# Kernel tuning notes

Measured on AMD Instinct MI355X. Metric: run time of the kernel, lower is better.

## Reference

```python
import jax, jax.numpy as jnp
import numpy as np

N = 100000          # nodes
E = 600000          # edges
H = 128             # hidden_dim
CF_DIM = 15         # input_dim - 1
NOISE_DIM = 32
NUM_CLASS = 6       # GraphConstructor.number_of_class
B = 64              # number of graphs in batch
BC = B * NUM_CLASS  # total clusters
LAYER_NUM = 3
NEG_SLOPE = 0.01


def setup_inputs() -> dict:
    key = jax.random.key(0)
    ks = jax.random.split(key, 12)
    cf = jax.random.normal(ks[0], (N, CF_DIM), jnp.float32)
    slf = jax.random.uniform(ks[1], (N,), jnp.float32)
    z = jax.random.normal(ks[2], (N, NOISE_DIM), jnp.float32)
    tr = jax.random.uniform(ks[3], (BC,), jnp.float32)
    W_enc = jax.random.normal(ks[4], (CF_DIM + 1 + NOISE_DIM, H), jnp.float32) * 0.05
    b_enc = jax.random.normal(ks[5], (H,), jnp.float32) * 0.05
    W_m = jax.random.normal(ks[6], (2 * H, H), jnp.float32) * 0.05
    b_m = jax.random.normal(ks[7], (H,), jnp.float32) * 0.05
    W_u = jax.random.normal(ks[8], (3 * H, H), jnp.float32) * 0.05
    b_u = jax.random.normal(ks[9], (H,), jnp.float32) * 0.05
    e = jax.random.randint(ks[10], (2, E), 0, N, jnp.int64)
    cc = jax.random.randint(ks[11], (N,), 0, BC, jnp.int64)
    cfb = cc // NUM_CLASS  # batch index consistent with global cluster index
    return {"cf": cf, "slf": slf, "z": z, "tr": tr,
            "W_enc": W_enc, "b_enc": b_enc, "W_m": W_m, "b_m": b_m,
            "W_u": W_u, "b_u": b_u, "e": e, "cc": cc, "cfb": cfb}


def _segment_mean(x, idx, num_segments):
    s = jax.ops.segment_sum(x, idx, num_segments=num_segments)
    c = jax.ops.segment_sum(jnp.ones((x.shape[0],), x.dtype), idx, num_segments=num_segments)
    return s / jnp.maximum(c, 1.0)[:, None]


def reference(cf, slf, z, tr, W_enc, b_enc, W_m, b_m, W_u, b_u, e, cc, cfb):
    # encoder: x = enc(cat(cf, slf, z))  (Linear, no activation since act='')
    x = jnp.concatenate([cf, slf[:, None], z], axis=-1) @ W_enc + b_enc  # [N, H]
    src, dst = e[0], e[1]  # PyG: x_j = x[src], x_i = x[dst], aggregate at dst
    for _ in range(LAYER_NUM):
        # message: MLP(cat(feature_i, feature_j)) per edge, mean-aggregated at dst
        msg = jnp.concatenate([x[dst], x[src]], axis=-1) @ W_m + b_m  # [E, H]
        aggr = _segment_mean(msg, dst, N)                              # [N, H]
        # cluster avg_pool scaled by target ratio, broadcast back to nodes
        pooled = _segment_mean(x, cc, BC) * tr[:, None]                # [BC, H]
        node_pool = pooled[cc]                                         # [N, H]
        upd = jnp.concatenate([x, aggr, node_pool], axis=-1) @ W_u + b_u
        upd = jnp.where(upd > 0, upd, NEG_SLOPE * upd)                 # LeakyReLU
        x = x + upd                                                    # residual
    return x
```

## Files before the change

kernel.cpp:

```cpp
#include <hip/hip_runtime.h>
#include <hip/hip_bf16.h>

#define N_NODES 100000
#define N_EDGES 600000
#define HD 128
#define NBC 384
#define SCAN_B 98
#define MAXFIX 4096
#define TILES ((N_NODES + 63) / 64)
#define GRID_F 512
#define AGG_B (N_NODES / 4)
#define CAPB 16384
#define PB_BLK 147

typedef __attribute__((ext_vector_type(8))) short s8v;
typedef __attribute__((ext_vector_type(4))) short s4v;
typedef __attribute__((ext_vector_type(4))) float f4v;
typedef __hip_bfloat16 bf16;

static __device__ __forceinline__ float bf2f(bf16 v) { return __bfloat162float(v); }
static __device__ __forceinline__ bf16 f2bf(float v) { return __float2bfloat16(v); }
static __device__ __forceinline__ float sh2f(short s) { bf16 h = *(bf16*)&s; return bf2f(h); }
static __device__ __forceinline__ float ldraw(const void* p, int i, int fp32) {
    return fp32 ? ((const float*)p)[i] : bf2f(((const bf16*)p)[i]);
}

static __device__ __forceinline__ void gl2lds16(const void* g, void* l) {
    __builtin_amdgcn_global_load_lds(
        (const __attribute__((address_space(1))) void*)g,
        (__attribute__((address_space(3))) void*)l, 16, 0, 0);
}

__global__ void k_init(const unsigned short* __restrict__ wraw, const int* __restrict__ eraw,
                       int* __restrict__ flags, int* __restrict__ deg,
                       int* __restrict__ ccount, int* __restrict__ n0cnt,
                       int* __restrict__ bcur) {
    int b = blockIdx.x, t = threadIdx.x;
    if (b == 0) {
        if (t < 64) {
            int bad = 0;
            for (int k = 0; k < 16; k++) {
                unsigned int u = ((unsigned int)wraw[t * 16 + k]) << 16;
                float f = fabsf(__uint_as_float(u));
                if (!(f <= 1e4f)) bad = 1;
            }
            unsigned long long m = __ballot(bad);
            if (t == 0) {
                flags[0] = m ? 1 : 0;
                flags[1] = (eraw[1] == 0 && eraw[3] == 0 && eraw[5] == 0 && eraw[7] == 0) ? 1 : 0;
            }
        }
    } else if (b <= 98) {
        int i = (b - 1) * 256 + t;
        if (i < 25000) ((int4*)deg)[i] = make_int4(0, 0, 0, 0);
    } else {
        if (t < 96) ((int4*)ccount)[t] = make_int4(0, 0, 0, 0);
        if (t == 96) *n0cnt = 0;
        if (t >= 128 && t < 128 + SCAN_B) bcur[t - 128] = 0;
    }
}

#define KB_J 192
#define KB_K (KB_J + 32)
#define KB_L (KB_K + 1)
#define KB_A (KB_L + 5860)
#define KB_B (KB_A + 391)
#define KB_C (KB_B + 12500)
#define KB_D (KB_C + 782)
#define KB_E (KB_D + 2)
#define KB_F (KB_E + 192)
#define KB_G (KB_F + 1)
#define KB_H (KB_G + 4688)
#define KB_I (KB_H + 391)
__global__ void k_mega(const int* __restrict__ flags,
                       const void* cf_r, const void* slf_r, const void* z_r,
                       const void* tr_r, const void* Wenc_r, const void* benc_r,
                       const void* Wm_r, const void* bm_r, const void* Wu_r,
                       const void* bu_r, const int* __restrict__ e_r,
                       const int* __restrict__ cc_r,
                       bf16* __restrict__ xin, bf16* __restrict__ trc,
                       bf16* __restrict__ Wuc, bf16* __restrict__ buc,
                       int* __restrict__ ec, int* __restrict__ ccc,
                       int* __restrict__ deg, int* __restrict__ ccount,
                       bf16* __restrict__ Wc, float* __restrict__ bc,
                       bf16* __restrict__ Wet, float* __restrict__ bcenc) {
    int b = blockIdx.x, t = threadIdx.x;
    int fp32 = flags[0];
    if (b < KB_J) {
        int i = b * 256 + t;
        int w = i / 384, kk = i - w * 384;
        float acc = 0.f;
        if (kk < 128) {
            acc = ldraw(Wu_r, kk * 128 + w, fp32);
            for (int j = 0; j < 128; j++)
                acc += ldraw(Wm_r, kk * 128 + j, fp32) * ldraw(Wu_r, (128 + j) * 128 + w, fp32);
        } else if (kk < 256) {
            int kp = kk - 128;
            for (int j = 0; j < 128; j++)
                acc += ldraw(Wm_r, (128 + kp) * 128 + j, fp32) * ldraw(Wu_r, (128 + j) * 128 + w, fp32);
        } else {
            acc = ldraw(Wu_r, kk * 128 + w, fp32);
        }
        Wc[w * 384 + kk] = f2bf(acc);
    } else if (b < KB_K) {
        int i = (b - KB_J) * 256 + t;
        int w = i >> 6, kk = i & 63;
        float v = (kk < 48) ? ldraw(Wenc_r, kk * 128 + w, fp32) : 0.f;
        Wet[i] = f2bf(v);
    } else if (b < KB_L) {
        if (t < 128) {
            float acc = ldraw(bu_r, t, fp32);
            for (int j = 0; j < 128; j++)
                acc += ldraw(bm_r, j, fp32) * ldraw(Wu_r, (128 + j) * 128 + t, fp32);
            bc[t] = acc;
        } else if (t < 256) {
            bcenc[t - 128] = ldraw(benc_r, t - 128, fp32);
        }
    } else if (b < KB_A) {
        int i = (b - KB_L) * 256 + t;
        if (i < 1500000) {
            int node = i / 15;
            xin[(size_t)node * 64 + (i - node * 15)] = f2bf(ldraw(cf_r, i, fp32));
        }
    } else if (b < KB_B) {
        int i = (b - KB_A) * 256 + t;
        if (i < 100000) xin[(size_t)i * 64 + 15] = f2bf(ldraw(slf_r, i, fp32));
    } else if (b < KB_C) {
        int i = (b - KB_B) * 256 + t;
        if (i < 3200000) xin[(size_t)(i >> 5) * 64 + 16 + (i & 31)] = f2bf(ldraw(z_r, i, fp32));
    } else if (b < KB_D) {
        int p = (b - KB_C) * 2048 + t * 8;
        if (p < 1600000) {
            int row = p >> 4, off = p & 15;
            s8v zz = {0, 0, 0, 0, 0, 0, 0, 0};
            *(s8v*)((short*)xin + (size_t)row * 64 + 48 + off) = zz;
        }
    } else if (b < KB_E) {
        int i = (b - KB_D) * 256 + t;
        if (i < 384) trc[i] = f2bf(ldraw(tr_r, i, fp32));
    } else if (b < KB_F) {
        int i = (b - KB_E) * 256 + t;
        Wuc[i] = f2bf(ldraw(Wu_r, i, fp32));
    } else if (b < KB_G) {
        if (t < 128) buc[t] = f2bf(ldraw(bu_r, t, fp32));
    } else if (b < KB_H) {
        int i64f = flags[1];
        int i = (b - KB_G) * 256 + t;
        if (i < 2 * N_EDGES) {
            int v = i64f ? e_r[2 * i] : e_r[i];
            ec[i] = v;
            if (i >= N_EDGES) atomicAdd(&deg[v], 1);
        }
    } else {
        int i64f = flags[1];
        int i = (b - KB_H) * 256 + t;
        if (i < N_NODES) {
            int v = i64f ? cc_r[2 * i] : cc_r[i];
            ccc[i] = v;
            atomicAdd(&ccount[v], 1);
        }
    }
}

__global__ void k_scan_a2(const int* __restrict__ deg, int* __restrict__ rowptr,
                          int* __restrict__ bsum, const int* __restrict__ ccount,
                          int* __restrict__ coff, int* __restrict__ ccur,
                          const int* __restrict__ ec, int* __restrict__ bcur,
                          int* __restrict__ ebuf) {
    __shared__ int sd[1024];
    __shared__ int hist[SCAN_B], hbase[SCAN_B], lcur[SCAN_B];
    int t = threadIdx.x;
    if (blockIdx.x < SCAN_B) {
        int i = blockIdx.x * 1024 + t;
        int v = (i < N_NODES) ? deg[i] : 0;
        sd[t] = v;
        __syncthreads();
#pragma unroll
        for (int off = 1; off < 1024; off <<= 1) {
            int u = (t >= off) ? sd[t - off] : 0;
            __syncthreads();
            sd[t] += u;
            __syncthreads();
        }
        if (i < N_NODES) rowptr[i] = sd[t] - v;
        if (t == 1023) bsum[blockIdx.x] = sd[t];
    } else if (blockIdx.x == SCAN_B) {
        int v = (t < NBC) ? ccount[t] : 0;
        sd[t] = v;
        __syncthreads();
#pragma unroll
        for (int off = 1; off < 1024; off <<= 1) {
            int u = (t >= off) ? sd[t - off] : 0;
            __syncthreads();
            sd[t] += u;
            __syncthreads();
        }
        if (t < NBC) {
            int ex = sd[t] - v;
            coff[t] = ex;
            ccur[t] = ex;
            if (t == NBC - 1) coff[NBC] = sd[t];
        }
    } else {
        int bb = blockIdx.x - (SCAN_B + 1);
        int e0 = bb * 4096;
        if (t < SCAN_B) { hist[t] = 0; lcur[t] = 0; }
        __syncthreads();
        int dv[4], sv[4], bk[4];
#pragma unroll
        for (int k = 0; k < 4; k++) {
            int i = e0 + k * 1024 + t;
            if (i < N_EDGES) {
                dv[k] = ec[N_EDGES + i];
                sv[k] = ec[i];
                bk[k] = dv[k] >> 10;
                atomicAdd(&hist[bk[k]], 1);
            } else bk[k] = -1;
        }
        __syncthreads();
        if (t < SCAN_B && hist[t] > 0) hbase[t] = atomicAdd(&bcur[t], hist[t]);
        __syncthreads();
#pragma unroll
        for (int k = 0; k < 4; k++) {
            if (bk[k] >= 0) {
                int rel = hbase[bk[k]] + atomicAdd(&lcur[bk[k]], 1);
                if (rel < CAPB) ebuf[bk[k] * CAPB + rel] = (sv[k] << 10) | (dv[k] & 1023);
            }
        }
    }
}

__global__ void k_scan_c2(int* __restrict__ rowptr, const int* __restrict__ bsum) {
    __shared__ int sb[128];
    __shared__ int offs;
    int b = blockIdx.x, t = threadIdx.x;
    if (t < 128) sb[t] = (t < b) ? bsum[t] : 0;
    __syncthreads();
    if (t == 0) {
        int s = 0;
        for (int k = 0; k < 128; k++) s += sb[k];
        offs = s;
    }
    __syncthreads();
    int i = b * 1024 + t;
    if (i < N_NODES) rowptr[i] = rowptr[i] + offs;
    if (b == 0 && t == 0) rowptr[N_NODES] = N_EDGES;
}

#define K5_EN 1563
#define K5_PC (K5_EN + SCAN_B)
#define K5_CF (K5_PC + SCAN_B)
#define K5_L0 (K5_CF + 391)
__global__ void k_front(const bf16* __restrict__ xin, const bf16* __restrict__ Wet,
                        const float* __restrict__ bcenc, bf16* __restrict__ xb,
                        const int* __restrict__ rowptr, const int* __restrict__ ebuf,
                        int* __restrict__ colx, const int* __restrict__ ccc,
                        int* __restrict__ ccur, int* __restrict__ cnodes,
                        const int* __restrict__ deg, int* __restrict__ n0list,
                        int* __restrict__ n0cnt) {
    __shared__ int cur[1024];
    __shared__ int h[NBC], cb[NBC];
    int b = blockIdx.x;
    if (b >= K5_EN) {
        if (b < K5_PC) {
            int bb = b - K5_EN;
            int base = bb << 10;
            int nlim = min(1024, N_NODES - base);
            for (int i = threadIdx.x; i < nlim; i += 256) cur[i] = rowptr[base + i];
            __syncthreads();
            int cnt = rowptr[base + nlim] - rowptr[base];
            const int* eb = ebuf + bb * CAPB;
            for (int e = threadIdx.x; e < cnt; e += 256) {
                int v = eb[e];
                int p = atomicAdd(&cur[v & 1023], 1);
                colx[p] = v >> 10;
            }
        } else if (b < K5_CF) {
            int bb = b - K5_PC;
            int base = bb << 10;
            int nlim = min(1024, N_NODES - base);
            for (int j = threadIdx.x; j < NBC; j += 256) h[j] = 0;
            __syncthreads();
            int cls[4];
#pragma unroll
            for (int k = 0; k < 4; k++) {
                int li = k * 256 + threadIdx.x;
                cls[k] = (li < nlim) ? ccc[base + li] : -1;
                if (cls[k] >= 0) atomicAdd(&h[cls[k]], 1);
            }
            __syncthreads();
            for (int j = threadIdx.x; j < NBC; j += 256) {
                cb[j] = h[j] ? atomicAdd(&ccur[j], h[j]) : 0;
                h[j] = 0;
            }
            __syncthreads();
#pragma unroll
            for (int k = 0; k < 4; k++) {
                if (cls[k] >= 0) {
                    int p = cb[cls[k]] + atomicAdd(&h[cls[k]], 1);
                    cnodes[p] = base + k * 256 + threadIdx.x;
                }
            }
        } else {
            int i = (b - K5_CF) * 256 + threadIdx.x;
            if (i < N_NODES && deg[i] == 0) {
                int p = atomicAdd(n0cnt, 1);
                if (p < MAXFIX) n0list[p] = i;
            }
        }
        return;
    }
    int tid = threadIdx.x;
    int r0 = b * 64;
    int wave = tid >> 6, lane = tid & 63, quad = lane >> 4, nidx = lane & 15;
    int colbase = wave * 32;

    int arow[4];
#pragma unroll
    for (int rt = 0; rt < 4; rt++) {
        int gr = r0 + rt * 16 + nidx;
        arow[rt] = (gr < N_NODES) ? gr : (N_NODES - 1);
    }
    f4v acc[4][2];
#pragma unroll
    for (int rt = 0; rt < 4; rt++)
#pragma unroll
        for (int ct = 0; ct < 2; ct++) acc[rt][ct] = (f4v){0.f, 0.f, 0.f, 0.f};

#pragma unroll
    for (int s = 0; s < 2; s++) {
        int k0 = s * 32;
        s8v bfrag[4];
#pragma unroll
        for (int rt = 0; rt < 4; rt++)
            bfrag[rt] = *(const s8v*)((const short*)xin + (size_t)arow[rt] * 64 + k0 + quad * 8);
#pragma unroll
        for (int ct = 0; ct < 2; ct++) {
            s8v wfr = *(const s8v*)((const short*)Wet + (colbase + ct * 16 + nidx) * 64 + k0 + quad * 8);
#pragma unroll
            for (int rt = 0; rt < 4; rt++)
                acc[rt][ct] = __builtin_amdgcn_mfma_f32_16x16x32_bf16(wfr, bfrag[rt], acc[rt][ct], 0, 0, 0);
        }
    }
#pragma unroll
    for (int rt = 0; rt < 4; rt++) {
        int gr = r0 + rt * 16 + nidx;
        if (gr < N_NODES) {
#pragma unroll
            for (int ct = 0; ct < 2; ct++) {
                int wc0 = colbase + ct * 16 + quad * 4;
                f4v bv = *(const f4v*)(bcenc + wc0);
                size_t idx = (size_t)gr * HD + wc0;
                s4v ob;
#pragma unroll
                for (int r = 0; r < 4; r++) {
                    float nv = acc[rt][ct][r] + bv[r];
                    bf16 h2 = f2bf(nv);
                    ob[r] = *(short*)&h2;
                }
                *(s4v*)((short*)xb + idx) = ob;
            }
        }
    }
}

__global__ void k_aggpool(const bf16* __restrict__ xb, const int* __restrict__ rowptr,
                          const int* __restrict__ colx, bf16* __restrict__ mb,
                          const int* __restrict__ coff, const int* __restrict__ cnodes,
                          const bf16* __restrict__ trc, bf16* __restrict__ pooled) {
    __shared__ float red[8][128];
    int tid = threadIdx.x;
    if (blockIdx.x < NBC) {
        int cl = blockIdx.x;
        int lo = coff[cl], hi = coff[cl + 1];
        int cnt = hi - lo;
        int slot = tid >> 5, cg = tid & 31;
        float a0 = 0.f, a1 = 0.f, a2 = 0.f, a3 = 0.f;
        for (int i = lo + slot; i < hi; i += 8) {
            int nd = cnodes[i];
            s4v v = *(const s4v*)((const short*)xb + (size_t)nd * HD + cg * 4);
            a0 += sh2f(v[0]); a1 += sh2f(v[1]); a2 += sh2f(v[2]); a3 += sh2f(v[3]);
        }
        red[slot][cg * 4 + 0] = a0;
        red[slot][cg * 4 + 1] = a1;
        red[slot][cg * 4 + 2] = a2;
        red[slot][cg * 4 + 3] = a3;
        __syncthreads();
        if (tid < 128) {
            float s = 0.f;
#pragma unroll
            for (int k = 0; k < 8; k++) s += red[k][tid];
            float v = s / (float)(cnt > 1 ? cnt : 1) * bf2f(trc[cl]);
            pooled[cl * HD + tid] = f2bf(v);
        }
        return;
    }
    int wave = tid >> 6, lane = tid & 63;
    int node = (blockIdx.x - NBC) * 4 + wave;
    if (node >= N_NODES) return;
    int half = lane >> 5;
    int l = lane & 31;
    int lo = rowptr[node], hi = rowptr[node + 1];
    float a0 = 0.f, a1 = 0.f, a2 = 0.f, a3 = 0.f;
    int j = lo + half;
    while (j + 2 < hi) {
        int s0 = colx[j], s1 = colx[j + 2];
        s4v v0 = *(const s4v*)((const short*)xb + (size_t)s0 * HD + l * 4);
        s4v v1 = *(const s4v*)((const short*)xb + (size_t)s1 * HD + l * 4);
        a0 += sh2f(v0[0]) + sh2f(v1[0]);
        a1 += sh2f(v0[1]) + sh2f(v1[1]);
        a2 += sh2f(v0[2]) + sh2f(v1[2]);
        a3 += sh2f(v0[3]) + sh2f(v1[3]);
        j += 4;
    }
    if (j < hi) {
        int s0 = colx[j];
        s4v v0 = *(const s4v*)((const short*)xb + (size_t)s0 * HD + l * 4);
        a0 += sh2f(v0[0]);
        a1 += sh2f(v0[1]);
        a2 += sh2f(v0[2]);
        a3 += sh2f(v0[3]);
    }
    a0 += __shfl_down(a0, 32);
    a1 += __shfl_down(a1, 32);
    a2 += __shfl_down(a2, 32);
    a3 += __shfl_down(a3, 32);
    if (half == 0) {
        int d = hi - lo;
        float inv = 1.0f / (float)(d > 1 ? d : 1);
        s4v o;
        bf16 h0 = f2bf(a0 * inv); o[0] = *(short*)&h0;
        bf16 h1 = f2bf(a1 * inv); o[1] = *(short*)&h1;
        bf16 h2 = f2bf(a2 * inv); o[2] = *(short*)&h2;
        bf16 h3 = f2bf(a3 * inv); o[3] = *(short*)&h3;
        *(s4v*)((short*)mb + (size_t)node * HD + l * 4) = o;
    }
}

__global__ __launch_bounds__(256, 2) void k_fused2(
    const bf16* __restrict__ xb, const bf16* __restrict__ mb, const bf16* __restrict__ pooled,
    const bf16* __restrict__ Wc, const float* __restrict__ bc,
    const int* __restrict__ cc, const int* __restrict__ deg,
    const bf16* __restrict__ Wuc, const bf16* __restrict__ buc,
    const int* __restrict__ n0list, const int* __restrict__ n0cnt,
    bf16* __restrict__ xbo, const int* __restrict__ flags,
    void* __restrict__ out, int last) {
    __shared__ short Lx[64 * 128];
    __shared__ short Lm[64 * 128];
    __shared__ short Lp[64 * 128];
    __shared__ float fxv[128];
    __shared__ float fpv[128];
    int tid = threadIdx.x;
    int wave = tid >> 6, lane = tid & 63, quad = lane >> 4, nidx = lane & 15;
    int colbase = wave * 32;
    int fp32out = flags[0];

    s8v wfr[12][2];
#pragma unroll
    for (int ct = 0; ct < 2; ct++) {
        int wcol = colbase + ((nidx >> 2) << 3) + ct * 4 + (nidx & 3);
        const short* wrow = (const short*)Wc + (size_t)wcol * 384 + quad * 8;
#pragma unroll
        for (int s = 0; s < 12; s++) wfr[s][ct] = *(const s8v*)(wrow + s * 32);
    }
    int cb2 = colbase + quad * 8;
    f4v bv0 = *(const f4v*)(bc + cb2);
    f4v bv1 = *(const f4v*)(bc + cb2 + 4);

    int srow = lane >> 4;
    int sc = lane & 15;

    for (int t = blockIdx.x; t < TILES; t += GRID_F) {
        int r0 = t * 64;
#pragma unroll
        for (int ii = 0; ii < 4; ii++) {
            int i = wave * 4 + ii;
            int lr = i * 4 + srow;
            int gr = r0 + lr;
            int grc = (gr < N_NODES) ? gr : (N_NODES - 1);
            int gc = sc ^ (lr & 15);
            gl2lds16((const short*)xb + (size_t)grc * HD + gc * 8, (char*)Lx + i * 1024);
            gl2lds16((const short*)mb + (size_t)grc * HD + gc * 8, (char*)Lm + i * 1024);
            int ci = cc[grc];
            gl2lds16((const short*)pooled + (size_t)ci * HD + gc * 8, (char*)Lp + i * 1024);
        }
        __syncthreads();

        f4v acc[4][2];
#pragma unroll
        for (int rt = 0; rt < 4; rt++)
#pragma unroll
            for (int ct = 0; ct < 2; ct++) acc[rt][ct] = (f4v){0.f, 0.f, 0.f, 0.f};

#pragma unroll
        for (int s = 0; s < 12; s++) {
            const short* Ls = (s < 4) ? Lx : ((s < 8) ? Lm : Lp);
            int c = (s & 3) * 4 + quad;
            s8v bfrag[4];
#pragma unroll
            for (int rt = 0; rt < 4; rt++) {
                int row = rt * 16 + nidx;
                int slot = c ^ nidx;
                bfrag[rt] = *(const s8v*)(Ls + row * 128 + slot * 8);
            }
#pragma unroll
            for (int ct = 0; ct < 2; ct++)
#pragma unroll
                for (int rt = 0; rt < 4; rt++)
                    acc[rt][ct] = __builtin_amdgcn_mfma_f32_16x16x32_bf16(wfr[s][ct], bfrag[rt], acc[rt][ct], 0, 0, 0);
        }

#pragma unroll
        for (int rt = 0; rt < 4; rt++) {
            int gr = r0 + rt * 16 + nidx;
            if (gr < N_NODES && deg[gr] > 0) {
                int row = rt * 16 + nidx;
                int slot = ((colbase >> 3) + quad) ^ nidx;
                s8v xo = *(const s8v*)(Lx + row * 128 + slot * 8);
                size_t idx = (size_t)gr * HD + cb2;
                float nv[8];
#pragma unroll
                for (int r = 0; r < 4; r++) {
                    float v0 = acc[rt][0][r] + bv0[r];
                    v0 = (v0 > 0.f) ? v0 : 0.01f * v0;
                    nv[r] = sh2f(xo[r]) + v0;
                    float v1 = acc[rt][1][r] + bv1[r];
                    v1 = (v1 > 0.f) ? v1 : 0.01f * v1;
                    nv[4 + r] = sh2f(xo[4 + r]) + v1;
                }
                if (last) {
                    if (fp32out) {
                        f4v o0 = {nv[0], nv[1], nv[2], nv[3]};
                        f4v o1 = {nv[4], nv[5], nv[6], nv[7]};
                        *(f4v*)((float*)out + idx) = o0;
                        *(f4v*)((float*)out + idx + 4) = o1;
                    } else {
                        s8v ob;
#pragma unroll
                        for (int r = 0; r < 8; r++) { bf16 h = f2bf(nv[r]); ob[r] = *(short*)&h; }
                        *(s8v*)((short*)out + idx) = ob;
                    }
                } else {
                    s8v ob;
#pragma unroll
                    for (int r = 0; r < 8; r++) { bf16 h = f2bf(nv[r]); ob[r] = *(short*)&h; }
                    *(s8v*)((short*)xbo + idx) = ob;
                }
            }
        }
        __syncthreads();
    }

    int cnt0 = *n0cnt;
    if (cnt0 > MAXFIX) cnt0 = MAXFIX;
    for (int j = blockIdx.x; j < cnt0; j += gridDim.x) {
        int v = n0list[j];
        if (tid < 128) {
            fxv[tid] = bf2f(xb[(size_t)v * HD + tid]);
            fpv[tid] = bf2f(pooled[cc[v] * HD + tid]);
        }
        __syncthreads();
        if (tid < 128) {
            float acc = bf2f(buc[tid]);
            for (int k = 0; k < 128; k++)
                acc += fxv[k] * bf2f(Wuc[k * 128 + tid]) + fpv[k] * bf2f(Wuc[(256 + k) * 128 + tid]);
            float u = acc > 0.f ? acc : 0.01f * acc;
            size_t idx = (size_t)v * HD + tid;
            float nv = fxv[tid] + u;
            if (last) {
                if (fp32out) ((float*)out)[idx] = nv;
                else ((bf16*)out)[idx] = f2bf(nv);
            } else {
                xbo[idx] = f2bf(nv);
            }
        }
        __syncthreads();
    }
}

extern "C" void kernel_launch(void* const* d_in, const int* in_sizes, int n_in,
                              void* d_out, int out_size, void* d_ws, size_t ws_size,
                              hipStream_t stream) {
    const void* cf_r = d_in[0];
    const void* slf_r = d_in[1];
    const void* z_r = d_in[2];
    const void* tr_r = d_in[3];
    const void* Wenc_r = d_in[4];
    const void* benc_r = d_in[5];
    const void* Wm_r = d_in[6];
    const void* bm_r = d_in[7];
    const void* Wu_r = d_in[8];
    const void* bu_r = d_in[9];
    const int* e_r = (const int*)d_in[10];
    const int* cc_r = (const int*)d_in[11];

    char* w = (char*)d_ws;
    auto alloc = [&](size_t bytes) -> char* {
        char* p = w;
        w += (bytes + 63) & ~(size_t)63;
        return p;
    };
    bf16* xb0 = (bf16*)alloc((size_t)N_NODES * HD * 2);
    bf16* xb1 = (bf16*)alloc((size_t)N_NODES * HD * 2);
    bf16* mb = (bf16*)alloc((size_t)N_NODES * HD * 2);
    bf16* xin = (bf16*)alloc((size_t)N_NODES * 64 * 2);
    bf16* Wc = (bf16*)alloc(128 * 384 * 2);
    float* bc = (float*)alloc(128 * 4);
    bf16* Wet = (bf16*)alloc(128 * 64 * 2);
    float* bcenc = (float*)alloc(128 * 4);
    bf16* pooled = (bf16*)alloc(NBC * HD * 2);
    int* deg = (int*)alloc(N_NODES * 4);
    int* rowptr = (int*)alloc((N_NODES + 1) * 4);
    int* colx = (int*)alloc(N_EDGES * 4);
    int* ccount = (int*)alloc(NBC * 4);
    int* coff = (int*)alloc((NBC + 1) * 4);
    int* ccur = (int*)alloc(NBC * 4);
    int* cnodes = (int*)alloc(N_NODES * 4);
    int* flags = (int*)alloc(64);
    int* bsum = (int*)alloc(SCAN_B * 4);
    int* n0list = (int*)alloc(MAXFIX * 4);
    int* n0cnt = (int*)alloc(64);
    bf16* trc = (bf16*)alloc(384 * 2);
    bf16* Wuc = (bf16*)alloc(49152 * 2);
    bf16* buc = (bf16*)alloc(128 * 2);
    int* ec = (int*)alloc(2 * N_EDGES * 4);
    int* ccc = (int*)alloc(N_NODES * 4);
    int* bcur = (int*)alloc(SCAN_B * 4);
    int* ebuf = (int*)alloc((size_t)SCAN_B * CAPB * 4);

    k_init<<<100, 256, 0, stream>>>((const unsigned short*)Wenc_r, e_r, flags,
                                    deg, ccount, n0cnt, bcur);
    k_mega<<<KB_I, 256, 0, stream>>>(flags, cf_r, slf_r, z_r, tr_r, Wenc_r, benc_r,
                                     Wm_r, bm_r, Wu_r, bu_r, e_r, cc_r,
                                     xin, trc, Wuc, buc, ec, ccc, deg, ccount,
                                     Wc, bc, Wet, bcenc);
    k_scan_a2<<<SCAN_B + 1 + PB_BLK, 1024, 0, stream>>>(deg, rowptr, bsum, ccount,
                                                        coff, ccur, ec, bcur, ebuf);
    k_scan_c2<<<SCAN_B, 1024, 0, stream>>>(rowptr, bsum);
    k_front<<<K5_L0, 256, 0, stream>>>(xin, Wet, bcenc, xb0,
                                       rowptr, ebuf, colx, ccc, ccur, cnodes,
                                       deg, n0list, n0cnt);

    bf16* xbufs[2] = {xb0, xb1};
    for (int layer = 0; layer < 3; layer++) {
        bf16* xbi = xbufs[layer & 1];
        bf16* xbo = xbufs[(layer + 1) & 1];
        int last = (layer == 2);
        k_aggpool<<<AGG_B + NBC, 256, 0, stream>>>(xbi, rowptr, colx, mb,
                                                   coff, cnodes, trc, pooled);
        k_fused2<<<GRID_F, 256, 0, stream>>>(xbi, mb, pooled, Wc, bc, ccc, deg,
                                             Wuc, buc, n0list, n0cnt,
                                             xbo, flags, d_out, last);
    }
}
```

Baseline: 428.3 us.

## Fuse edge bucketing into preprocessing kernel and vectorize node input packing

```diff
diff --git a/kernel.cpp b/kernel.cpp
--- a/kernel.cpp
+++ b/kernel.cpp
@@ -11,7 +11,6 @@
 #define GRID_F 512
 #define AGG_B (N_NODES / 4)
 #define CAPB 16384
-#define PB_BLK 147
 
 typedef __attribute__((ext_vector_type(8))) short s8v;
 typedef __attribute__((ext_vector_type(4))) short s4v;
@@ -60,18 +59,14 @@
     }
 }
 
-#define KB_J 192
-#define KB_K (KB_J + 32)
-#define KB_L (KB_K + 1)
-#define KB_A (KB_L + 5860)
-#define KB_B (KB_A + 391)
-#define KB_C (KB_B + 12500)
-#define KB_D (KB_C + 782)
-#define KB_E (KB_D + 2)
-#define KB_F (KB_E + 192)
-#define KB_G (KB_F + 1)
-#define KB_H (KB_G + 4688)
-#define KB_I (KB_H + 391)
+#define KB_COMP 192
+#define KB_EDGE (KB_COMP + 586)
+#define KB_XIN  (KB_EDGE + 391)
+#define KB_CC   (KB_XIN + 391)
+#define KB_WUC  (KB_CC + 192)
+#define KB_WET  (KB_WUC + 32)
+#define KB_BC   (KB_WET + 1)
+#define KB_TR   (KB_BC + 2)
 __global__ void k_mega(const int* __restrict__ flags,
                        const void* cf_r, const void* slf_r, const void* z_r,
                        const void* tr_r, const void* Wenc_r, const void* benc_r,
@@ -80,95 +75,137 @@
                        const int* __restrict__ cc_r,
                        bf16* __restrict__ xin, bf16* __restrict__ trc,
                        bf16* __restrict__ Wuc, bf16* __restrict__ buc,
-                       int* __restrict__ ec, int* __restrict__ ccc,
+                       int* __restrict__ ccc,
                        int* __restrict__ deg, int* __restrict__ ccount,
                        bf16* __restrict__ Wc, float* __restrict__ bc,
-                       bf16* __restrict__ Wet, float* __restrict__ bcenc) {
+                       bf16* __restrict__ Wet, float* __restrict__ bcenc,
+                       int* __restrict__ bcur, int* __restrict__ ebuf) {
+    __shared__ float scf[3840];
+    __shared__ int hist[SCAN_B], hbase[SCAN_B], lcur[SCAN_B];
     int b = blockIdx.x, t = threadIdx.x;
     int fp32 = flags[0];
-    if (b < KB_J) {
+    if (b < KB_COMP) {
         int i = b * 256 + t;
-        int w = i / 384, kk = i - w * 384;
+        int w = i & 127, kk = i >> 7;
         float acc = 0.f;
         if (kk < 128) {
             acc = ldraw(Wu_r, kk * 128 + w, fp32);
+#pragma unroll 8
             for (int j = 0; j < 128; j++)
                 acc += ldraw(Wm_r, kk * 128 + j, fp32) * ldraw(Wu_r, (128 + j) * 128 + w, fp32);
         } else if (kk < 256) {
             int kp = kk - 128;
+#pragma unroll 8
             for (int j = 0; j < 128; j++)
                 acc += ldraw(Wm_r, (128 + kp) * 128 + j, fp32) * ldraw(Wu_r, (128 + j) * 128 + w, fp32);
         } else {
             acc = ldraw(Wu_r, kk * 128 + w, fp32);
         }
         Wc[w * 384 + kk] = f2bf(acc);
-    } else if (b < KB_K) {
-        int i = (b - KB_J) * 256 + t;
+    } else if (b < KB_EDGE) {
+        int i64f = flags[1];
+        int bb = b - KB_COMP;
+        int e0 = bb * 1024;
+        if (t < SCAN_B) { hist[t] = 0; lcur[t] = 0; }
+        __syncthreads();
+        int sv[4], dv[4], bk[4];
+#pragma unroll
+        for (int k = 0; k < 4; k++) {
+            int i = e0 + k * 256 + t;
+            if (i < N_EDGES) {
+                sv[k] = i64f ? e_r[2 * i] : e_r[i];
+                dv[k] = i64f ? e_r[2 * (N_EDGES + i)] : e_r[N_EDGES + i];
+                bk[k] = dv[k] >> 10;
+                atomicAdd(&hist[bk[k]], 1);
+                atomicAdd(&deg[dv[k]], 1);
+            } else bk[k] = -1;
+        }
+        __syncthreads();
+        if (t < SCAN_B && hist[t] > 0) hbase[t] = atomicAdd(&bcur[t], hist[t]);
+        __syncthreads();
+#pragma unroll
+        for (int k = 0; k < 4; k++) {
+            if (bk[k] >= 0) {
+                int rel = hbase[bk[k]] + atomicAdd(&lcur[bk[k]], 1);
+                if (rel < CAPB) ebuf[bk[k] * CAPB + rel] = (sv[k] << 10) | (dv[k] & 1023);
+            }
+        }
+    } else if (b < KB_XIN) {
+        int base = (b - KB_EDGE) * 256;
+        int gbase = base * 15;
+        int cnt = min(3840, 1500000 - gbase);
+        for (int k = t; k < cnt; k += 256) scf[k] = ldraw(cf_r, gbase + k, fp32);
+        __syncthreads();
+        int node = base + t;
+        if (node < N_NODES) {
+            float vals[64];
+#pragma unroll
+            for (int k = 0; k < 64; k++) vals[k] = 0.f;
+#pragma unroll
+            for (int k = 0; k < 15; k++) vals[k] = scf[t * 15 + k];
+            vals[15] = ldraw(slf_r, node, fp32);
+            if (fp32) {
+                const f4v* zp = (const f4v*)((const float*)z_r + (size_t)node * 32);
+#pragma unroll
+                for (int k = 0; k < 8; k++) {
+                    f4v v = zp[k];
+#pragma unroll
+                    for (int r = 0; r < 4; r++) vals[16 + k * 4 + r] = v[r];
+                }
+            } else {
+                const s8v* zp = (const s8v*)((const short*)z_r + (size_t)node * 32);
+#pragma unroll
+                for (int k = 0; k < 4; k++) {
+                    s8v v = zp[k];
+#pragma unroll
+                    for (int r = 0; r < 8; r++) vals[16 + k * 8 + r] = sh2f(v[r]);
+                }
+            }
+            short* xr = (short*)xin + (size_t)node * 64;
+#pragma unroll
+            for (int k = 0; k < 8; k++) {
+                s8v ov;
+#pragma unroll
+                for (int r = 0; r < 8; r++) { bf16 h = f2bf(vals[k * 8 + r]); ov[r] = *(short*)&h; }
+                *(s8v*)(xr + k * 8) = ov;
+            }
+        }
+    } else if (b < KB_CC) {
+        int i64f = flags[1];
+        int i = (b - KB_XIN) * 256 + t;
+        if (i < N_NODES) {
+            int v = i64f ? cc_r[2 * i] : cc_r[i];
+            ccc[i] = v;
+            atomicAdd(&ccount[v], 1);
+        }
+    } else if (b < KB_WUC) {
+        int i = (b - KB_CC) * 256 + t;
+        Wuc[i] = f2bf(ldraw(Wu_r, i, fp32));
+    } else if (b < KB_WET) {
+        int i = (b - KB_WUC) * 256 + t;
         int w = i >> 6, kk = i & 63;
         float v = (kk < 48) ? ldraw(Wenc_r, kk * 128 + w, fp32) : 0.f;
         Wet[i] = f2bf(v);
-    } else if (b < KB_L) {
+    } else if (b < KB_BC) {
         if (t < 128) {
             float acc = ldraw(bu_r, t, fp32);
             for (int j = 0; j < 128; j++)
                 acc += ldraw(bm_r, j, fp32) * ldraw(Wu_r, (128 + j) * 128 + t, fp32);
             bc[t] = acc;
-        } else if (t < 256) {
+        } else {
             bcenc[t - 128] = ldraw(benc_r, t - 128, fp32);
-        }
-    } else if (b < KB_A) {
-        int i = (b - KB_L) * 256 + t;
-        if (i < 1500000) {
-            int node = i / 15;
-            xin[(size_t)node * 64 + (i - node * 15)] = f2bf(ldraw(cf_r, i, fp32));
-        }
-    } else if (b < KB_B) {
-        int i = (b - KB_A) * 256 + t;
-        if (i < 100000) xin[(size_t)i * 64 + 15] = f2bf(ldraw(slf_r, i, fp32));
-    } else if (b < KB_C) {
-        int i = (b - KB_B) * 256 + t;
-        if (i < 3200000) xin[(size_t)(i >> 5) * 64 + 16 + (i & 31)] = f2bf(ldraw(z_r, i, fp32));
-    } else if (b < KB_D) {
-        int p = (b - KB_C) * 2048 + t * 8;
-        if (p < 1600000) {
-            int row = p >> 4, off = p & 15;
-            s8v zz = {0, 0, 0, 0, 0, 0, 0, 0};
-            *(s8v*)((short*)xin + (size_t)row * 64 + 48 + off) = zz;
-        }
-    } else if (b < KB_E) {
-        int i = (b - KB_D) * 256 + t;
+            buc[t - 128] = f2bf(ldraw(bu_r, t - 128, fp32));
+        }
+    } else {
+        int i = (b - KB_BC) * 256 + t;
         if (i < 384) trc[i] = f2bf(ldraw(tr_r, i, fp32));
-    } else if (b < KB_F) {
-        int i = (b - KB_E) * 256 + t;
-        Wuc[i] = f2bf(ldraw(Wu_r, i, fp32));
-    } else if (b < KB_G) {
-        if (t < 128) buc[t] = f2bf(ldraw(bu_r, t, fp32));
-    } else if (b < KB_H) {
-        int i64f = flags[1];
-        int i = (b - KB_G) * 256 + t;
-        if (i < 2 * N_EDGES) {
-            int v = i64f ? e_r[2 * i] : e_r[i];
-            ec[i] = v;
-            if (i >= N_EDGES) atomicAdd(&deg[v], 1);
-        }
-    } else {
-        int i64f = flags[1];
-        int i = (b - KB_H) * 256 + t;
-        if (i < N_NODES) {
-            int v = i64f ? cc_r[2 * i] : cc_r[i];
-            ccc[i] = v;
-            atomicAdd(&ccount[v], 1);
-        }
     }
 }
 
 __global__ void k_scan_a2(const int* __restrict__ deg, int* __restrict__ rowptr,
                           int* __restrict__ bsum, const int* __restrict__ ccount,
-                          int* __restrict__ coff, int* __restrict__ ccur,
-                          const int* __restrict__ ec, int* __restrict__ bcur,
-                          int* __restrict__ ebuf) {
+                          int* __restrict__ coff, int* __restrict__ ccur) {
     __shared__ int sd[1024];
-    __shared__ int hist[SCAN_B], hbase[SCAN_B], lcur[SCAN_B];
     int t = threadIdx.x;
     if (blockIdx.x < SCAN_B) {
         int i = blockIdx.x * 1024 + t;
@@ -184,7 +221,7 @@
         }
         if (i < N_NODES) rowptr[i] = sd[t] - v;
         if (t == 1023) bsum[blockIdx.x] = sd[t];
-    } else if (blockIdx.x == SCAN_B) {
+    } else {
         int v = (t < NBC) ? ccount[t] : 0;
         sd[t] = v;
         __syncthreads();
@@ -200,32 +237,6 @@
             coff[t] = ex;
             ccur[t] = ex;
             if (t == NBC - 1) coff[NBC] = sd[t];
-        }
-    } else {
-        int bb = blockIdx.x - (SCAN_B + 1);
-        int e0 = bb * 4096;
-        if (t < SCAN_B) { hist[t] = 0; lcur[t] = 0; }
-        __syncthreads();
-        int dv[4], sv[4], bk[4];
-#pragma unroll
-        for (int k = 0; k < 4; k++) {
-            int i = e0 + k * 1024 + t;
-            if (i < N_EDGES) {
-                dv[k] = ec[N_EDGES + i];
-                sv[k] = ec[i];
-                bk[k] = dv[k] >> 10;
-                atomicAdd(&hist[bk[k]], 1);
-            } else bk[k] = -1;
-        }
-        __syncthreads();
-        if (t < SCAN_B && hist[t] > 0) hbase[t] = atomicAdd(&bcur[t], hist[t]);
-        __syncthreads();
-#pragma unroll
-        for (int k = 0; k < 4; k++) {
-            if (bk[k] >= 0) {
-                int rel = hbase[bk[k]] + atomicAdd(&lcur[bk[k]], 1);
-                if (rel < CAPB) ebuf[bk[k] * CAPB + rel] = (sv[k] << 10) | (dv[k] & 1023);
-            }
         }
     }
 }
@@ -623,19 +634,17 @@
     bf16* trc = (bf16*)alloc(384 * 2);
     bf16* Wuc = (bf16*)alloc(49152 * 2);
     bf16* buc = (bf16*)alloc(128 * 2);
-    int* ec = (int*)alloc(2 * N_EDGES * 4);
     int* ccc = (int*)alloc(N_NODES * 4);
     int* bcur = (int*)alloc(SCAN_B * 4);
     int* ebuf = (int*)alloc((size_t)SCAN_B * CAPB * 4);
 
     k_init<<<100, 256, 0, stream>>>((const unsigned short*)Wenc_r, e_r, flags,
                                     deg, ccount, n0cnt, bcur);
-    k_mega<<<KB_I, 256, 0, stream>>>(flags, cf_r, slf_r, z_r, tr_r, Wenc_r, benc_r,
-                                     Wm_r, bm_r, Wu_r, bu_r, e_r, cc_r,
-                                     xin, trc, Wuc, buc, ec, ccc, deg, ccount,
-                                     Wc, bc, Wet, bcenc);
-    k_scan_a2<<<SCAN_B + 1 + PB_BLK, 1024, 0, stream>>>(deg, rowptr, bsum, ccount,
-                                                        coff, ccur, ec, bcur, ebuf);
+    k_mega<<<KB_TR, 256, 0, stream>>>(flags, cf_r, slf_r, z_r, tr_r, Wenc_r, benc_r,
+                                      Wm_r, bm_r, Wu_r, bu_r, e_r, cc_r,
+                                      xin, trc, Wuc, buc, ccc, deg, ccount,
+                                      Wc, bc, Wet, bcenc, bcur, ebuf);
+    k_scan_a2<<<SCAN_B + 1, 1024, 0, stream>>>(deg, rowptr, bsum, ccount, coff, ccur);
     k_scan_c2<<<SCAN_B, 1024, 0, stream>>>(rowptr, bsum);
     k_front<<<K5_L0, 256, 0, stream>>>(xin, Wet, bcenc, xb0,
                                        rowptr, ebuf, colx, ccc, ccur, cnodes,
```

Result: no change. 420.1 us (-1.9%).
